# Performance work log

Hardware: AMD Instinct MI355X
Metric: run time of the kernel (lower is better)

## Reference

```python
import jax, jax.numpy as jnp
import numpy as np

DIM = 512
NUM_HEADS = 8
HEAD_DIM = DIM // NUM_HEADS
LOCAL_HEADS = 4
WINDOW = 64
NEG_INF = -1e9


def setup_inputs() -> dict:
    key = jax.random.key(0)
    ks = jax.random.split(key, 5)
    B, N, C = 4, 8192, DIM
    x = jax.random.normal(ks[0], (B, N, C), dtype=jnp.float32)
    # nn.Linear weights stored as [out, in]; xavier-ish scale
    s = (2.0 / (C + C)) ** 0.5
    Wq = jax.random.normal(ks[1], (C, C), dtype=jnp.float32) * s
    Wkv = jax.random.normal(ks[2], (C, C), dtype=jnp.float32) * s
    Wproj = jax.random.normal(ks[3], (C, C), dtype=jnp.float32) * s
    bproj = jax.random.normal(ks[4], (C,), dtype=jnp.float32) * 0.01
    return {"x": x, "Wq": Wq, "Wkv": Wkv, "Wproj": Wproj, "bproj": bproj}


def _look_around(t):
    # t: [B,H,nw,m,d] -> [B,H,nw,3m,d] (prev window, current, next; zero-padded at ends)
    p = jnp.pad(t, ((0, 0), (0, 0), (1, 1), (0, 0), (0, 0)))
    return jnp.concatenate([p[:, :, :-2], p[:, :, 1:-1], p[:, :, 2:]], axis=3)


def _local_attn(q, k, v, m):
    # non-causal LocalAttention, look_backward=1, look_forward=1
    B, H, N, d = q.shape
    nw = N // m
    scale = d ** -0.5
    qw = q.reshape(B, H, nw, m, d)
    kw = _look_around(k.reshape(B, H, nw, m, d))
    vw = _look_around(v.reshape(B, H, nw, m, d))
    # mask out look-around positions that fall outside the sequence
    pos = jnp.arange(N).reshape(nw, m)
    pp = jnp.pad(pos, ((1, 1), (0, 0)), constant_values=-1)
    kpos = jnp.concatenate([pp[:-2], pp[1:-1], pp[2:]], axis=1)  # [nw, 3m]
    valid = (kpos >= 0)[None, None, :, None, :]
    scores = jnp.einsum('bhwid,bhwjd->bhwij', qw * scale, kw)
    scores = jnp.where(valid, scores, NEG_INF)
    attn = jax.nn.softmax(scores, axis=-1)
    out = jnp.einsum('bhwij,bhwjd->bhwid', attn, vw)
    return out.reshape(B, H, N, d)


def _linear_attn(q, k, v):
    d = q.shape[-1]
    q = jax.nn.softmax(q, axis=-1) * (d ** -0.5)
    k = jax.nn.softmax(k, axis=-2)
    context = jnp.einsum('bhnd,bhne->bhde', k, v)
    return jnp.einsum('bhnd,bhde->bhne', q, context)


def reference(x, Wq, Wkv, Wproj, bproj):
    B, N, C = x.shape
    m = WINDOW
    original_N = N
    rem = N % m  # static; 0 for chosen shapes
    if rem > 0:
        x = jnp.pad(x, ((0, 0), (m - rem, 0), (0, 0)))
        N = x.shape[1]
    q = x @ Wq.T
    k = x @ Wkv.T
    v = x @ Wkv.T  # source uses the same kv linear for both k and v
    merge = lambda t: t.reshape(B, N, -1, HEAD_DIM).transpose(0, 2, 1, 3)  # [B,H,N,d]
    q, k, v = merge(q), merge(k), merge(v)
    lh = LOCAL_HEADS
    lq, gq = q[:, :lh], q[:, lh:]
    lk, gk = k[:, :lh], k[:, lh:]
    lv, gv = v[:, :lh], v[:, lh:]
    outs = []
    if lh > 0:
        outs.append(_local_attn(lq, lk, lv, m))
    if q.shape[1] - lh > 0:
        outs.append(_linear_attn(gq, gk, gv))
    attn = jnp.concatenate(outs, axis=1)  # [B,H,N,d]
    y = attn.transpose(0, 2, 1, 3).reshape(B, N, -1)
    y = y[:, -original_N:]
    y = y @ Wproj.T + bproj
    return (y, attn)
```

## Files before the change

### kernel.cpp

```cpp
#include <hip/hip_runtime.h>

#define DIM 512
#define NH 8
#define HD 64
#define LH 4
#define WIN 64
#define BATCH 4
#define SEQ 8192
#define NWIN (SEQ/WIN)

typedef unsigned short u16;
typedef __bf16 bf16x8 __attribute__((ext_vector_type(8)));
typedef float f32x4 __attribute__((ext_vector_type(4)));

__device__ __forceinline__ float b2f(u16 u) {
    return __uint_as_float(((unsigned int)u) << 16);
}
__device__ __forceinline__ u16 f2b(float f) {
    unsigned int x = __float_as_uint(f);
    return (u16)((x + 0x7FFFu + ((x >> 16) & 1u)) >> 16);
}

__device__ __forceinline__ void gload16(const void* g, void* l) {
    __builtin_amdgcn_global_load_lds(
        (__attribute__((address_space(1))) void*)g,
        (__attribute__((address_space(3))) void*)l, 16, 0, 0);
}

__global__ void convert_bf16(const float* __restrict__ src, u16* __restrict__ dst, long n)
{
    long i = ((long)blockIdx.x * 256 + threadIdx.x) * 8;
    const long stride = (long)gridDim.x * 256 * 8;
    for (; i < n; i += stride) {
        uint4 a = *(const uint4*)(src + i), b = *(const uint4*)(src + i + 4);
        const float* af = (const float*)&a;
        const float* bf_ = (const float*)&b;
        uint4 o; u16* ou = (u16*)&o;
        #pragma unroll
        for (int j = 0; j < 4; j++) { ou[j] = f2b(af[j]); ou[4 + j] = f2b(bf_[j]); }
        *(uint4*)(dst + i) = o;
    }
}

__global__ __launch_bounds__(256) void gemm_qk_tiled(const u16* __restrict__ xb,
        const u16* __restrict__ Wqk, u16* __restrict__ qh, u16* __restrict__ kh)
{
    __shared__ __align__(16) u16 smem[16384];
    u16* lA = smem;
    u16* lB = smem + 4096;

    const int tid = threadIdx.x;
    const int wv = tid >> 6, lane = tid & 63;
    const int quad = lane >> 4, l16 = lane & 15;
    const int wr = wv >> 1, wc = wv & 1;
    const int row0 = blockIdx.y * 128;
    const int col0 = blockIdx.x * 128;
    const int lrow = lane >> 2, lkc = (lane & 3) * 8;

    f32x4 acc[4][4];
    #pragma unroll
    for (int t = 0; t < 4; t++)
        for (int u = 0; u < 4; u++)
            for (int i = 0; i < 4; i++) acc[t][u][i] = 0.f;

    const u16* gA = xb  + (size_t)(row0 + lrow) * DIM + lkc;
    const u16* gB = Wqk + (size_t)(col0 + lrow) * DIM + lkc;

    for (int kt = 0; kt < DIM; kt += 32) {
        __syncthreads();
        #pragma unroll
        for (int i = 0; i < 2; i++) {
            int rb = wv * 32 + i * 16;
            gload16(gA + (size_t)rb * DIM + kt, &lA[rb * 32]);
            gload16(gB + (size_t)rb * DIM + kt, &lB[rb * 32]);
        }
        __syncthreads();
        bf16x8 af[4], bfr[4];
        #pragma unroll
        for (int t = 0; t < 4; t++)
            af[t] = *(const bf16x8*)&lA[(wr * 64 + t * 16 + l16) * 32 + quad * 8];
        #pragma unroll
        for (int u = 0; u < 4; u++)
            bfr[u] = *(const bf16x8*)&lB[(wc * 64 + u * 16 + l16) * 32 + quad * 8];
        #pragma unroll
        for (int t = 0; t < 4; t++)
            #pragma unroll
            for (int u = 0; u < 4; u++)
                acc[t][u] = __builtin_amdgcn_mfma_f32_16x16x32_bf16(af[t], bfr[u], acc[t][u], 0, 0, 0);
    }

    __syncthreads();
    u16* cw = smem + wv * 4096;
    #pragma unroll
    for (int t = 0; t < 4; t++)
        #pragma unroll
        for (int u = 0; u < 4; u++)
            #pragma unroll
            for (int r = 0; r < 4; r++)
                cw[(t * 16 + quad * 4 + r) * 64 + u * 16 + l16] = f2b(acc[t][u][r]);

    const int colg0 = col0 + wc * 64;
    const int seg = lane & 7;
    u16* dstbase;
    {
        int h = (colg0 & 511) >> 6;
        u16* base = (colg0 < 512) ? qh : kh;
        dstbase = base + (size_t)h * SEQ * HD;
    }
    #pragma unroll
    for (int i = 0; i < 8; i++) {
        int mm = i * 8 + (lane >> 3);
        uint4 v = *(const uint4*)&cw[mm * 64 + seg * 8];
        int m = row0 + wr * 64 + mm;
        int bb = m >> 13, nn = m & (SEQ - 1);
        *(uint4*)(dstbase + ((size_t)bb * NH * SEQ + nn) * HD + seg * 8) = v;
    }
}

#define KJ_STRIDE 72
#define KT_STRIDE 200

__global__ __launch_bounds__(256) void local_attn(const u16* __restrict__ qh,
        const u16* __restrict__ kh, float* __restrict__ attn_out)
{
    __shared__ __align__(16) u16 kjP[192 * KJ_STRIDE];
    __shared__ __align__(16) u16 kT[64 * KT_STRIDE];

    const int w = blockIdx.x;
    const int bh = blockIdx.y;
    const int b = bh >> 2, h = bh & 3;
    const int tid = threadIdx.x;
    const int wv = tid >> 6, lane = tid & 63;
    const int quad = lane >> 4, l16 = lane & 15;

    for (int idx = tid; idx < 192 * 8; idx += 256) {
        int j = idx >> 3, dc = (idx & 7) << 3;
        int n = w * WIN - WIN + j;
        uint4 val = make_uint4(0, 0, 0, 0);
        if (n >= 0 && n < SEQ)
            val = *(const uint4*)(kh + (((size_t)(b * NH + h)) * SEQ + n) * HD + dc);
        *(uint4*)(&kjP[j * KJ_STRIDE + dc]) = val;
    }
    __syncthreads();
    for (int idx = tid; idx < 64 * 192; idx += 256) {
        int e = idx & 63, j = idx >> 6;
        kT[e * KT_STRIDE + j] = kjP[j * KJ_STRIDE + e];
    }
    __syncthreads();

    f32x4 s[12];
    #pragma unroll
    for (int t = 0; t < 12; t++)
        for (int i = 0; i < 4; i++) s[t][i] = 0.f;

    const u16* qrow = qh + (((size_t)(b * NH + h)) * SEQ + w * WIN + wv * 16 + l16) * HD + quad * 8;
    #pragma unroll
    for (int kk = 0; kk < 64; kk += 32) {
        bf16x8 a = *(const bf16x8*)(qrow + kk);
        #pragma unroll
        for (int t = 0; t < 12; t++) {
            bf16x8 bf = *(const bf16x8*)(&kjP[(t * 16 + l16) * KJ_STRIDE + kk + quad * 8]);
            s[t] = __builtin_amdgcn_mfma_f32_16x16x32_bf16(a, bf, s[t], 0, 0, 0);
        }
    }
    __syncthreads();

    const float scale = 0.125f;
    #pragma unroll
    for (int r = 0; r < 4; r++) {
        float vals[12];
        float mx = -3.0e38f;
        #pragma unroll
        for (int t = 0; t < 12; t++) {
            int j = t * 16 + l16;
            float v = s[t][r] * scale;
            bool valid = !((w == 0 && j < 64) || (w == NWIN - 1 && j >= 128));
            v = valid ? v : -30000.0f;
            vals[t] = v;
            mx = fmaxf(mx, v);
        }
        for (int m = 1; m <= 8; m <<= 1) mx = fmaxf(mx, __shfl_xor(mx, m));
        float sum = 0.f;
        #pragma unroll
        for (int t = 0; t < 12; t++) { vals[t] = __expf(vals[t] - mx); sum += vals[t]; }
        for (int m = 1; m <= 8; m <<= 1) sum += __shfl_xor(sum, m);
        float inv = 1.0f / sum;
        int prow = wv * 16 + quad * 4 + r;
        #pragma unroll
        for (int t = 0; t < 12; t++)
            kjP[prow * KT_STRIDE + t * 16 + l16] = f2b(vals[t] * inv);
    }
    __syncthreads();

    f32x4 o[4];
    #pragma unroll
    for (int t = 0; t < 4; t++)
        for (int i = 0; i < 4; i++) o[t][i] = 0.f;
    #pragma unroll
    for (int kc = 0; kc < 6; kc++) {
        bf16x8 a = *(const bf16x8*)(&kjP[(wv * 16 + l16) * KT_STRIDE + kc * 32 + quad * 8]);
        #pragma unroll
        for (int t = 0; t < 4; t++) {
            bf16x8 bf = *(const bf16x8*)(&kT[(t * 16 + l16) * KT_STRIDE + kc * 32 + quad * 8]);
            o[t] = __builtin_amdgcn_mfma_f32_16x16x32_bf16(a, bf, o[t], 0, 0, 0);
        }
    }
    #pragma unroll
    for (int t = 0; t < 4; t++) {
        int e = t * 16 + l16;
        #pragma unroll
        for (int r = 0; r < 4; r++) {
            int n = w * WIN + wv * 16 + quad * 4 + r;
            attn_out[(((size_t)(b * NH + h)) * SEQ + n) * HD + e] = o[t][r];
        }
    }
}

__global__ __launch_bounds__(256) void ctx_accum(const u16* __restrict__ kh,
        float* __restrict__ partials, float* __restrict__ colsum)
{
    const int chunk = blockIdx.x;
    const int bh = blockIdx.y;
    const int b = bh >> 2, hg = bh & 3;
    const int tid = threadIdx.x;
    const int wv = tid >> 6, lane = tid & 63;
    const int d0 = (lane >> 2) * 4;
    const int e0 = (lane & 3) * 16;

    __shared__ __align__(16) float smem[2 * 64 * 68];
    float* kraw = smem;
    float* kexp = smem + 64 * 68;

    f32x4 acc[4][4];
    #pragma unroll
    for (int dd = 0; dd < 4; dd++)
        #pragma unroll
        for (int j = 0; j < 4; j++)
            for (int i = 0; i < 4; i++) acc[dd][j][i] = 0.f;
    f32x4 csum;
    for (int i = 0; i < 4; i++) csum[i] = 0.f;

    const u16* kbase = kh + ((size_t)(b * NH + LH + hg)) * SEQ * HD
                          + (size_t)chunk * 256 * HD;

    for (int ph = 0; ph < 4; ph++) {
        __syncthreads();
        #pragma unroll
        for (int pass = 0; pass < 2; pass++) {
            int idx = pass * 256 + tid;
            int row = idx >> 3, seg = (idx & 7) * 8;
            uint4 v = *(const uint4*)(kbase + ((size_t)(ph * 64 + row)) * HD + seg);
            const u16* u = (const u16*)&v;
            f32x4 r0, r1, E0, E1;
            #pragma unroll
            for (int j = 0; j < 4; j++) {
                r0[j] = b2f(u[j]);      E0[j] = __expf(r0[j]);
                r1[j] = b2f(u[4 + j]);  E1[j] = __expf(r1[j]);
            }
            float* kr = &kraw[row * 68 + seg];
            float* ke = &kexp[row * 68 + seg];
            *(f32x4*)kr = r0;  *(f32x4*)(kr + 4) = r1;
            *(f32x4*)ke = E0;  *(f32x4*)(ke + 4) = E1;
        }
        __syncthreads();
        #pragma unroll 4
        for (int i = 0; i < 16; i++) {
            int roff = (wv * 16 + i) * 68;
            f32x4 ek = *(const f32x4*)&kexp[roff + d0];
            const f32x4* kv = (const f32x4*)&kraw[roff + e0];
            f32x4 k0 = kv[0], k1 = kv[1], k2 = kv[2], k3 = kv[3];
            csum += ek;
            #pragma unroll
            for (int dd = 0; dd < 4; dd++) {
                acc[dd][0] += ek[dd] * k0;
                acc[dd][1] += ek[dd] * k1;
                acc[dd][2] += ek[dd] * k2;
                acc[dd][3] += ek[dd] * k3;
            }
        }
    }

    float* red0 = smem;
    float* red1 = smem + 4160;
    __syncthreads();
    if (wv >= 2) {
        float* rd = (wv == 2) ? red0 : red1;
        #pragma unroll
        for (int dd = 0; dd < 4; dd++)
            #pragma unroll
            for (int j = 0; j < 4; j++)
                *(f32x4*)&rd[(d0 + dd) * 64 + e0 + j * 4] = acc[dd][j];
        if ((lane & 3) == 0) *(f32x4*)&rd[4096 + d0] = csum;
    }
    __syncthreads();
    if (wv < 2) {
        float* rd = (wv == 0) ? red0 : red1;
        #pragma unroll
        for (int dd = 0; dd < 4; dd++)
            #pragma unroll
            for (int j = 0; j < 4; j++)
                acc[dd][j] += *(const f32x4*)&rd[(d0 + dd) * 64 + e0 + j * 4];
        csum += *(const f32x4*)&rd[4096 + d0];
    }
    __syncthreads();
    if (wv == 1) {
        #pragma unroll
        for (int dd = 0; dd < 4; dd++)
            #pragma unroll
            for (int j = 0; j < 4; j++)
                *(f32x4*)&red0[(d0 + dd) * 64 + e0 + j * 4] = acc[dd][j];
        if ((lane & 3) == 0) *(f32x4*)&red0[4096 + d0] = csum;
    }
    __syncthreads();
    if (wv == 0) {
        float* P = partials + ((size_t)(chunk * 16 + bh)) * 4096;
        #pragma unroll
        for (int dd = 0; dd < 4; dd++)
            #pragma unroll
            for (int j = 0; j < 4; j++) {
                f32x4 r = acc[dd][j] + *(const f32x4*)&red0[(d0 + dd) * 64 + e0 + j * 4];
                *(f32x4*)&P[(d0 + dd) * 64 + e0 + j * 4] = r;
            }
        if ((lane & 3) == 0) {
            f32x4 cs = csum + *(const f32x4*)&red0[4096 + d0];
            #pragma unroll
            for (int dd = 0; dd < 4; dd++)
                atomicAdd(colsum + bh * 64 + d0 + dd, cs[dd]);
        }
    }
}

__global__ __launch_bounds__(256) void reduce_ctx(const float* __restrict__ partials,
        const float* __restrict__ colsum, float* __restrict__ ctx)
{
    const int quarter = blockIdx.x;
    const int bh = blockIdx.y;
    const int tid = threadIdx.x;
    __shared__ float cs[64];
    if (tid < 64) cs[tid] = colsum[bh * 64 + tid];
    __syncthreads();
    const int i0 = quarter * 1024;
    for (int idx = i0 + tid; idx < i0 + 1024; idx += 256) {
        float s = 0.f;
        #pragma unroll 8
        for (int c = 0; c < 32; c++)
            s += partials[((size_t)(c * 16 + bh)) * 4096 + idx];
        ctx[(size_t)bh * 4096 + idx] = s / cs[idx >> 6];
    }
}

__global__ __launch_bounds__(256) void global_out(const u16* __restrict__ qh,
        const float* __restrict__ ctxg, float* __restrict__ attn_out)
{
    const int nblk = blockIdx.x;
    const int bh = blockIdx.y;
    const int b = bh >> 2, hg = bh & 3;
    const int tid = threadIdx.x;

    __shared__ float ctx[4096];
    for (int idx = tid; idx < 4096; idx += 256)
        ctx[idx] = ctxg[(size_t)bh * 4096 + idx];
    __syncthreads();

    const int n = nblk * 256 + tid;
    const size_t rowidx = (((size_t)(b * NH + LH + hg)) * SEQ + n) * HD;
    const u16* qrow = qh + rowidx;

    float sumexp = 0.f;
    for (int c = 0; c < 8; c++) {
        uint4 v = *(const uint4*)(qrow + c * 8);
        const u16* u = (const u16*)&v;
        #pragma unroll
        for (int jj = 0; jj < 8; jj++) sumexp += __expf(b2f(u[jj]));
    }
    float inv = 0.125f / sumexp;

    f32x4 out4[16];
    #pragma unroll
    for (int t = 0; t < 16; t++)
        for (int i = 0; i < 4; i++) out4[t][i] = 0.f;

    for (int c = 0; c < 8; c++) {
        uint4 v = *(const uint4*)(qrow + c * 8);
        const u16* u = (const u16*)&v;
        #pragma unroll
        for (int jj = 0; jj < 8; jj++) {
            float pd = __expf(b2f(u[jj])) * inv;
            const f32x4* cr = (const f32x4*)&ctx[(c * 8 + jj) * 64];
            #pragma unroll
            for (int t = 0; t < 16; t++)
                out4[t] += pd * cr[t];
        }
    }

    float* ao = attn_out + rowidx;
    #pragma unroll
    for (int t = 0; t < 16; t++)
        *(f32x4*)(ao + t * 4) = out4[t];
}

__global__ __launch_bounds__(256) void proj_gemm_tiled(const float* __restrict__ attn_out,
        const u16* __restrict__ Wproj, const float* __restrict__ bproj,
        float* __restrict__ y)
{
    __shared__ __align__(16) u16 smem[8192];
    u16* lA = smem;
    u16* lB = smem + 4096;

    const int tid = threadIdx.x;
    const int wv = tid >> 6, lane = tid & 63;
    const int quad = lane >> 4, l16 = lane & 15;
    const int wr = wv >> 1, wc = wv & 1;
    const int row0 = blockIdx.y * 128;
    const int col0 = blockIdx.x * 128;
    const int lrow = lane >> 2, lkc = (lane & 3) * 8;

    f32x4 acc[4][4];
    #pragma unroll
    for (int t = 0; t < 4; t++)
        for (int u = 0; u < 4; u++)
            for (int i = 0; i < 4; i++) acc[t][u][i] = 0.f;

    const u16* gB = Wproj + (size_t)(col0 + lrow) * DIM + lkc;

    for (int kt = 0; kt < DIM; kt += 32) {
        const int h = kt >> 6;
        const int e0 = (kt & 63) + lkc;
        __syncthreads();
        #pragma unroll
        for (int i = 0; i < 2; i++) {
            int rb = wv * 32 + i * 16;
            gload16(gB + (size_t)rb * DIM + kt, &lB[rb * 32]);
            int m = row0 + rb + lrow;
            int bb = m >> 13, nn = m & (SEQ - 1);
            const float* ga = attn_out + (((size_t)(bb * NH + h)) * SEQ + nn) * HD + e0;
            uint4 f0 = *(const uint4*)ga;
            uint4 f1 = *(const uint4*)(ga + 4);
            const float* a0 = (const float*)&f0;
            const float* a1 = (const float*)&f1;
            uint4 o; u16* ou = (u16*)&o;
            #pragma unroll
            for (int j = 0; j < 4; j++) { ou[j] = f2b(a0[j]); ou[4 + j] = f2b(a1[j]); }
            *(uint4*)&lA[(rb + lrow) * 32 + lkc] = o;
        }
        __syncthreads();
        bf16x8 af[4], bfr[4];
        #pragma unroll
        for (int t = 0; t < 4; t++)
            af[t] = *(const bf16x8*)&lA[(wr * 64 + t * 16 + l16) * 32 + quad * 8];
        #pragma unroll
        for (int u = 0; u < 4; u++)
            bfr[u] = *(const bf16x8*)&lB[(wc * 64 + u * 16 + l16) * 32 + quad * 8];
        #pragma unroll
        for (int t = 0; t < 4; t++)
            #pragma unroll
            for (int u = 0; u < 4; u++)
                acc[t][u] = __builtin_amdgcn_mfma_f32_16x16x32_bf16(af[t], bfr[u], acc[t][u], 0, 0, 0);
    }

    #pragma unroll
    for (int u = 0; u < 4; u++) {
        int col = col0 + wc * 64 + u * 16 + l16;
        float bias = bproj[col];
        #pragma unroll
        for (int t = 0; t < 4; t++)
            #pragma unroll
            for (int r = 0; r < 4; r++) {
                int m = row0 + wr * 64 + t * 16 + quad * 4 + r;
                y[(size_t)m * DIM + col] = acc[t][u][r] + bias;
            }
    }
}

extern "C" void kernel_launch(void* const* d_in, const int* in_sizes, int n_in,
                              void* d_out, int out_size, void* d_ws, size_t ws_size,
                              hipStream_t stream)
{
    (void)in_sizes; (void)n_in; (void)out_size; (void)ws_size;
    const float* x     = (const float*)d_in[0];
    const float* Wq    = (const float*)d_in[1];
    const float* Wkv   = (const float*)d_in[2];
    const float* Wproj = (const float*)d_in[3];
    const float* bproj = (const float*)d_in[4];

    float* y        = (float*)d_out;
    float* attn_out = y + (size_t)BATCH * SEQ * DIM;

    u16* xb = (u16*)y;
    u16* qh = xb + (size_t)BATCH * SEQ * DIM;

    float* partials = attn_out + (size_t)LH * SEQ * HD;

    char* ws = (char*)d_ws;
    float* S       = (float*)ws;
    float* colsum  = (float*)(ws + 262144);
    u16*   Wqk     = (u16*)(ws + 266240);
    u16*   Wproj_b = (u16*)(ws + 266240 + 1048576);
    u16*   kh      = (u16*)(ws + 266240 + 1048576 + 524288);

    const long NX = (long)BATCH * SEQ * DIM;
    const long NWT = (long)DIM * DIM;

    hipMemsetAsync(colsum, 0, 4096, stream);
    convert_bf16<<<4096, 256, 0, stream>>>(x, xb, NX);
    convert_bf16<<<128, 256, 0, stream>>>(Wq, Wqk, NWT);
    convert_bf16<<<128, 256, 0, stream>>>(Wkv, Wqk + NWT, NWT);
    convert_bf16<<<128, 256, 0, stream>>>(Wproj, Wproj_b, NWT);

    gemm_qk_tiled<<<dim3(8, 256), 256, 0, stream>>>(xb, Wqk, qh, kh);
    local_attn<<<dim3(NWIN, 16), 256, 0, stream>>>(qh, kh, attn_out);
    ctx_accum<<<dim3(32, 16), 256, 0, stream>>>(kh, partials, colsum);
    reduce_ctx<<<dim3(4, 16), 256, 0, stream>>>(partials, colsum, S);
    global_out<<<dim3(32, 16), 256, 0, stream>>>(qh, S, attn_out);
    proj_gemm_tiled<<<dim3(4, 256), 256, 0, stream>>>(attn_out, Wproj_b, bproj, y);
}
```

Baseline: 383.8 us.

## Emit bf16 token-major attention copy and feed projection GEMM via direct LDS loads

The local and global attention kernels now also write a bf16 copy of their output in [B,N,C] token-major layout. The projection GEMM can then stream its A operand with global_load_lds, instead of gathering fp32 head-major rows and converting them in registers. The three weight conversions are also merged into one launch. The cost is an extra bf16 write pass, an LDS transpose in local_attn, and more workspace.

```diff
diff --git a/kernel.cpp b/kernel.cpp
--- a/kernel.cpp
+++ b/kernel.cpp
@@ -42,6 +42,24 @@
     }
 }
 
+__global__ void convert_w3(const float* __restrict__ Wq, const float* __restrict__ Wkv,
+                           const float* __restrict__ Wp, u16* __restrict__ Wqk,
+                           u16* __restrict__ Wproj_b)
+{
+    const int slice = blockIdx.y;
+    const float* src = (slice == 0) ? Wq : (slice == 1) ? Wkv : Wp;
+    u16* dst = (slice == 0) ? Wqk : (slice == 1) ? (Wqk + DIM * DIM) : Wproj_b;
+    long i = ((long)blockIdx.x * 256 + threadIdx.x) * 8;
+    if (i >= (long)DIM * DIM) return;
+    uint4 a = *(const uint4*)(src + i), b = *(const uint4*)(src + i + 4);
+    const float* af = (const float*)&a;
+    const float* bf_ = (const float*)&b;
+    uint4 o; u16* ou = (u16*)&o;
+    #pragma unroll
+    for (int j = 0; j < 4; j++) { ou[j] = f2b(af[j]); ou[4 + j] = f2b(bf_[j]); }
+    *(uint4*)(dst + i) = o;
+}
+
 __global__ __launch_bounds__(256) void gemm_qk_tiled(const u16* __restrict__ xb,
         const u16* __restrict__ Wqk, u16* __restrict__ qh, u16* __restrict__ kh)
 {
@@ -119,9 +137,11 @@
 
 #define KJ_STRIDE 72
 #define KT_STRIDE 200
+#define OT_STRIDE 80
 
 __global__ __launch_bounds__(256) void local_attn(const u16* __restrict__ qh,
-        const u16* __restrict__ kh, float* __restrict__ attn_out)
+        const u16* __restrict__ kh, float* __restrict__ attn_out,
+        u16* __restrict__ attn_b)
 {
     __shared__ __align__(16) u16 kjP[192 * KJ_STRIDE];
     __shared__ __align__(16) u16 kT[64 * KT_STRIDE];
@@ -213,6 +233,18 @@
             int n = w * WIN + wv * 16 + quad * 4 + r;
             attn_out[(((size_t)(b * NH + h)) * SEQ + n) * HD + e] = o[t][r];
         }
+    }
+    __syncthreads();
+    #pragma unroll
+    for (int t = 0; t < 4; t++)
+        #pragma unroll
+        for (int r = 0; r < 4; r++)
+            kT[(wv * 16 + quad * 4 + r) * OT_STRIDE + t * 16 + l16] = f2b(o[t][r]);
+    __syncthreads();
+    for (int idx = tid; idx < 512; idx += 256) {
+        int row = idx >> 3, seg = (idx & 7) * 8;
+        uint4 v = *(const uint4*)&kT[row * OT_STRIDE + seg];
+        *(uint4*)(attn_b + ((size_t)(b * SEQ + w * WIN + row)) * DIM + h * HD + seg) = v;
     }
 }
 
@@ -350,7 +382,8 @@
 }
 
 __global__ __launch_bounds__(256) void global_out(const u16* __restrict__ qh,
-        const float* __restrict__ ctxg, float* __restrict__ attn_out)
+        const float* __restrict__ ctxg, float* __restrict__ attn_out,
+        u16* __restrict__ attn_b)
 {
     const int nblk = blockIdx.x;
     const int bh = blockIdx.y;
@@ -397,9 +430,18 @@
     #pragma unroll
     for (int t = 0; t < 16; t++)
         *(f32x4*)(ao + t * 4) = out4[t];
-}
-
-__global__ __launch_bounds__(256) void proj_gemm_tiled(const float* __restrict__ attn_out,
+
+    u16* ab = attn_b + ((size_t)(b * SEQ + n)) * DIM + (LH + hg) * HD;
+    #pragma unroll
+    for (int t = 0; t < 8; t++) {
+        uint4 o; u16* ou = (u16*)&o;
+        #pragma unroll
+        for (int j = 0; j < 8; j++) ou[j] = f2b(out4[t * 2 + (j >> 2)][j & 3]);
+        *(uint4*)(ab + t * 8) = o;
+    }
+}
+
+__global__ __launch_bounds__(256) void proj_gemm_tiled(const u16* __restrict__ attn_b,
         const u16* __restrict__ Wproj, const float* __restrict__ bproj,
         float* __restrict__ y)
 {
@@ -421,27 +463,16 @@
         for (int u = 0; u < 4; u++)
             for (int i = 0; i < 4; i++) acc[t][u][i] = 0.f;
 
-    const u16* gB = Wproj + (size_t)(col0 + lrow) * DIM + lkc;
+    const u16* gA = attn_b + (size_t)(row0 + lrow) * DIM + lkc;
+    const u16* gB = Wproj  + (size_t)(col0 + lrow) * DIM + lkc;
 
     for (int kt = 0; kt < DIM; kt += 32) {
-        const int h = kt >> 6;
-        const int e0 = (kt & 63) + lkc;
         __syncthreads();
         #pragma unroll
         for (int i = 0; i < 2; i++) {
             int rb = wv * 32 + i * 16;
+            gload16(gA + (size_t)rb * DIM + kt, &lA[rb * 32]);
             gload16(gB + (size_t)rb * DIM + kt, &lB[rb * 32]);
-            int m = row0 + rb + lrow;
-            int bb = m >> 13, nn = m & (SEQ - 1);
-            const float* ga = attn_out + (((size_t)(bb * NH + h)) * SEQ + nn) * HD + e0;
-            uint4 f0 = *(const uint4*)ga;
-            uint4 f1 = *(const uint4*)(ga + 4);
-            const float* a0 = (const float*)&f0;
-            const float* a1 = (const float*)&f1;
-            uint4 o; u16* ou = (u16*)&o;
-            #pragma unroll
-            for (int j = 0; j < 4; j++) { ou[j] = f2b(a0[j]); ou[4 + j] = f2b(a1[j]); }
-            *(uint4*)&lA[(rb + lrow) * 32 + lkc] = o;
         }
         __syncthreads();
         bf16x8 af[4], bfr[4];
@@ -497,20 +528,18 @@
     u16*   Wqk     = (u16*)(ws + 266240);
     u16*   Wproj_b = (u16*)(ws + 266240 + 1048576);
     u16*   kh      = (u16*)(ws + 266240 + 1048576 + 524288);
+    u16*   attn_b  = kh + (size_t)BATCH * SEQ * DIM;
 
     const long NX = (long)BATCH * SEQ * DIM;
-    const long NWT = (long)DIM * DIM;
 
     hipMemsetAsync(colsum, 0, 4096, stream);
     convert_bf16<<<4096, 256, 0, stream>>>(x, xb, NX);
-    convert_bf16<<<128, 256, 0, stream>>>(Wq, Wqk, NWT);
-    convert_bf16<<<128, 256, 0, stream>>>(Wkv, Wqk + NWT, NWT);
-    convert_bf16<<<128, 256, 0, stream>>>(Wproj, Wproj_b, NWT);
+    convert_w3<<<dim3(128, 3), 256, 0, stream>>>(Wq, Wkv, Wproj, Wqk, Wproj_b);
 
     gemm_qk_tiled<<<dim3(8, 256), 256, 0, stream>>>(xb, Wqk, qh, kh);
-    local_attn<<<dim3(NWIN, 16), 256, 0, stream>>>(qh, kh, attn_out);
+    local_attn<<<dim3(NWIN, 16), 256, 0, stream>>>(qh, kh, attn_out, attn_b);
     ctx_accum<<<dim3(32, 16), 256, 0, stream>>>(kh, partials, colsum);
     reduce_ctx<<<dim3(4, 16), 256, 0, stream>>>(partials, colsum, S);
-    global_out<<<dim3(32, 16), 256, 0, stream>>>(qh, S, attn_out);
-    proj_gemm_tiled<<<dim3(4, 256), 256, 0, stream>>>(attn_out, Wproj_b, bproj, y);
-}
+    global_out<<<dim3(32, 16), 256, 0, stream>>>(qh, S, attn_out, attn_b);
+    proj_gemm_tiled<<<dim3(4, 256), 256, 0, stream>>>(attn_b, Wproj_b, bproj, y);
+}
```

New measurement: 368.2 us. -4.1%, faster.
